# Kernel tuning notes

Measured on AMD Instinct MI355X. Metric: run time of the kernel, lower is better.

The kernel has to match this reference:

```python
import jax, jax.numpy as jnp
import numpy as np

EMBED_DIM = 1024
NUM_HEADS = 16
HEAD_DIM = EMBED_DIM // NUM_HEADS
BZ, Q_LEN, CACHE_LEN = 4, 512, 1536


def setup_inputs() -> dict:
    key = jax.random.key(0)
    ks = jax.random.split(key, 8)
    inp = {
        "hidden_states": jax.random.normal(ks[0], (BZ, Q_LEN, EMBED_DIM), jnp.float32),
        "attention_mask": jnp.zeros((BZ, 1, 1, CACHE_LEN + Q_LEN), jnp.float32),
        "k_cache": jax.random.normal(ks[1], (BZ, CACHE_LEN, EMBED_DIM), jnp.float32),
        "v_cache": jax.random.normal(ks[2], (BZ, CACHE_LEN, EMBED_DIM), jnp.float32),
        "Wq": jax.random.normal(ks[3], (EMBED_DIM, EMBED_DIM), jnp.float32) * 0.02,
        "bq": jnp.zeros((EMBED_DIM,), jnp.float32),
        "Wk": jax.random.normal(ks[4], (EMBED_DIM, EMBED_DIM), jnp.float32) * 0.02,
        "bk": jnp.zeros((EMBED_DIM,), jnp.float32),
        "Wv": jax.random.normal(ks[5], (EMBED_DIM, EMBED_DIM), jnp.float32) * 0.02,
        "bv": jnp.zeros((EMBED_DIM,), jnp.float32),
        "Wo": jax.random.normal(ks[6], (EMBED_DIM, EMBED_DIM), jnp.float32) * 0.02,
        "bo": jnp.zeros((EMBED_DIM,), jnp.float32),
    }
    return inp


def reference(hidden_states, attention_mask, k_cache, v_cache,
              Wq, bq, Wk, bk, Wv, bv, Wo, bo):
    bz, q_len, embed_dim = hidden_states.shape
    # projections (nn.Linear: x @ W.T + b)
    q = hidden_states @ Wq.T + bq
    k_new = hidden_states @ Wk.T + bk
    v_new = hidden_states @ Wv.T + bv
    # KV-cache concat (self_attn path)
    k = jnp.concatenate([k_cache, k_new], axis=1)  # [bz, kv_len, E]
    v = jnp.concatenate([v_cache, v_new], axis=1)
    q_begin = k_cache.shape[1]
    kv_len = k.shape[1]
    # split heads -> [bz, H, L, D]
    qh = q.reshape(bz, q_len, NUM_HEADS, HEAD_DIM).transpose(0, 2, 1, 3)
    kh = k.reshape(bz, kv_len, NUM_HEADS, HEAD_DIM).transpose(0, 2, 1, 3)
    vh = v.reshape(bz, kv_len, NUM_HEADS, HEAD_DIM).transpose(0, 2, 1, 3)
    scores = jnp.einsum("bhqd,bhkd->bhqk", qh, kh) / (HEAD_DIM ** 0.5)
    # causal mask slice causal_mask[q_begin:q_begin+q_len, :kv_len]
    rows = q_begin + jnp.arange(q_len)          # absolute query positions
    cols = jnp.arange(kv_len)
    causal = jnp.where(cols[None, :] > rows[:, None], -jnp.inf, 0.0).astype(scores.dtype)
    scores = scores + attention_mask + causal
    probs = jax.nn.softmax(scores, axis=-1)
    ctx = jnp.einsum("bhqk,bhkd->bhqd", probs, vh)
    ctx = ctx.transpose(0, 2, 1, 3).reshape(bz, q_len, embed_dim)
    out = ctx @ Wo.T + bo
    return out, k, v
```

## Files before the change

kernel.cpp:

```cpp
#include <hip/hip_runtime.h>
#include <hip/hip_bf16.h>
#include <stdint.h>

#define BZv 4
#define QL 512
#define CL 1536
#define KVL 2048
#define EMB 1024
#define NH 16
#define HD 64
#define QSCALE 0.18033688011112042f
#define NG 2048

typedef __attribute__((ext_vector_type(8))) short short8;
typedef __attribute__((ext_vector_type(4))) float floatx4;
typedef __attribute__((ext_vector_type(4))) float fx4;

__device__ __forceinline__ unsigned short f2b(float f) {
  union { float f; unsigned int u; } v; v.f = f;
  return (unsigned short)((v.u + 0x7FFFu + ((v.u >> 16) & 1u)) >> 16);
}

__device__ __forceinline__ ushort2 pk2(float a, float b) {
  union { __hip_bfloat162 h; ushort2 u; } c;
  c.h = __float22bfloat162_rn(make_float2(a, b));
  return c.u;
}

__device__ __forceinline__ short8 cvt8(fx4 a, fx4 b) {
  short8 r;
  r[0] = (short)f2b(a.x); r[1] = (short)f2b(a.y);
  r[2] = (short)f2b(a.z); r[3] = (short)f2b(a.w);
  r[4] = (short)f2b(b.x); r[5] = (short)f2b(b.y);
  r[6] = (short)f2b(b.z); r[7] = (short)f2b(b.w);
  return r;
}
__device__ __forceinline__ short8 cvt8w(fx4 a, fx4 b, float w) {
  short8 r;
  r[0] = (short)f2b(a.x * w); r[1] = (short)f2b(a.y * w);
  r[2] = (short)f2b(a.z * w); r[3] = (short)f2b(a.w * w);
  r[4] = (short)f2b(b.x * w); r[5] = (short)f2b(b.y * w);
  r[6] = (short)f2b(b.z * w); r[7] = (short)f2b(b.w * w);
  return r;
}

#if __has_builtin(__builtin_amdgcn_exp2f)
#define EXP2F(x) __builtin_amdgcn_exp2f(x)
#else
#define EXP2F(x) exp2f(x)
#endif

__device__ __forceinline__ void gload_lds16(const void* g, void* l) {
  __builtin_amdgcn_global_load_lds(
      (const __attribute__((address_space(1))) unsigned char*)g,
      (__attribute__((address_space(3))) unsigned char*)l, 16, 0, 0);
}

#define BAR_LIGHT() asm volatile("s_barrier" ::: "memory")
#define BAR_K() asm volatile("s_waitcnt vmcnt(3) lgkmcnt(0)\n\ts_barrier" ::: "memory")

__global__ __launch_bounds__(256) void prep_kernel(
    const float* __restrict__ hid, const float* __restrict__ Wq, const float* __restrict__ Wk,
    const float* __restrict__ Wv, const float* __restrict__ Wo,
    const float* __restrict__ kc, const float* __restrict__ vc, const float* __restrict__ msk,
    unsigned short* __restrict__ Xb, unsigned short* __restrict__ Wqb, unsigned short* __restrict__ Wkb,
    unsigned short* __restrict__ Wvb, unsigned short* __restrict__ Wob,
    unsigned short* __restrict__ Kb, unsigned short* __restrict__ Vb,
    float* __restrict__ kf, float* __restrict__ vf, unsigned short* __restrict__ wb)
{
  const int blk = blockIdx.x, tid = threadIdx.x;
  if (blk < 768) {
    const float* src; unsigned short* dst; int base;
    if (blk < 256) { src = hid; dst = Xb; base = blk * 2048; }
    else {
      int w = (blk - 256) >> 7, wo = (blk - 256) & 127;
      src = (w == 0) ? Wq : (w == 1) ? Wk : (w == 2) ? Wv : Wo;
      dst = (w == 0) ? Wqb : (w == 1) ? Wkb : (w == 2) ? Wvb : Wob;
      base = wo * 2048;
    }
    const fx4* s4 = (const fx4*)src;
    short8* d8 = (short8*)dst;
    fx4 v[8];
#pragma unroll
    for (int it = 0; it < 4; ++it) {
      int u = base + it * 512 + tid * 2;
      v[2 * it] = s4[u]; v[2 * it + 1] = s4[u + 1];
    }
#pragma unroll
    for (int it = 0; it < 4; ++it) {
      int u = base + it * 512 + tid * 2;
      d8[u >> 1] = cvt8(v[2 * it], v[2 * it + 1]);
    }
  } else if (blk < 1792) {
    const bool isV = blk >= 1280;
    const int r = blk - (isV ? 1280 : 768);
    const int bb = r >> 7, ko = r & 127;
    const fx4* s4 = (const fx4*)((isV ? vc : kc) + (long)bb * CL * EMB);
    fx4* f4 = (fx4*)((isV ? vf : kf) + (long)bb * KVL * EMB);
    short8* b8 = (short8*)((isV ? Vb : Kb) + (long)bb * KVL * EMB);
    const float* mrow = msk + bb * KVL;
    fx4 v[12];
#pragma unroll
    for (int it = 0; it < 6; ++it) {
      int u = ko * 3072 + it * 512 + tid * 2;
      v[2 * it] = s4[u]; v[2 * it + 1] = s4[u + 1];
    }
#pragma unroll
    for (int it = 0; it < 6; ++it) {
      int u = ko * 3072 + it * 512 + tid * 2;
      f4[u] = v[2 * it]; f4[u + 1] = v[2 * it + 1];
      if (isV) {
        float w = __expf(mrow[u >> 8]);
        b8[u >> 1] = cvt8w(v[2 * it], v[2 * it + 1], w);
      } else {
        b8[u >> 1] = cvt8(v[2 * it], v[2 * it + 1]);
      }
    }
  } else {
    const fx4* m4 = (const fx4*)msk;
    short8* w8 = (short8*)wb;
#pragma unroll
    for (int it = 0; it < 4; ++it) {
      int u = it * 512 + tid * 2;
      fx4 a = m4[u], b = m4[u + 1];
      fx4 ea, eb;
      ea.x = __expf(a.x); ea.y = __expf(a.y); ea.z = __expf(a.z); ea.w = __expf(a.w);
      eb.x = __expf(b.x); eb.y = __expf(b.y); eb.z = __expf(b.z); eb.w = __expf(b.w);
      w8[u >> 1] = cvt8(ea, eb);
    }
  }
}

__global__ __launch_bounds__(256) void qkv_gemm(
    const unsigned short* __restrict__ Xb,
    const unsigned short* __restrict__ Wqb, const unsigned short* __restrict__ Wkb,
    const unsigned short* __restrict__ Wvb,
    const float* __restrict__ bq, const float* __restrict__ bk, const float* __restrict__ bv,
    const float* __restrict__ msk,
    unsigned short* __restrict__ Qb, unsigned short* __restrict__ Kb, unsigned short* __restrict__ Vb,
    float* __restrict__ kf, float* __restrict__ vf)
{
  __shared__ unsigned short At[128 * 64];
  __shared__ unsigned short Bt[64 * 64];
  const int tid = threadIdx.x, lane = tid & 63, wave = tid >> 6;
  const int quad = lane >> 4, l = lane & 15;
  const int sw = l & 7;
  const int mat = blockIdx.x >> 4;
  const int ncol = (blockIdx.x & 15) * 64;
  const int mbase = blockIdx.y * 128;
  const unsigned short* W = (mat == 0) ? Wqb : (mat == 1) ? Wkb : Wvb;
  const float* bias = (mat == 0) ? bq : (mat == 1) ? bk : bv;
  const int rh = wave * 32;

  floatx4 zero = {0.f, 0.f, 0.f, 0.f};
  floatx4 acc[2][4];
#pragma unroll
  for (int i = 0; i < 2; i++)
#pragma unroll
    for (int j = 0; j < 4; j++) acc[i][j] = zero;

  for (int k0 = 0; k0 < EMB; k0 += 64) {
    if (k0) BAR_LIGHT();
#pragma unroll
    for (int s = 0; s < 4; s++) {
      int g = s * 256 + tid;
      int r = g >> 3, c = g & 7;
      gload_lds16(Xb + (size_t)(mbase + r) * EMB + k0 + ((c ^ (r & 7)) * 8), &At[g * 8]);
    }
#pragma unroll
    for (int s = 0; s < 2; s++) {
      int g = s * 256 + tid;
      int r = g >> 3, c = g & 7;
      gload_lds16(W + (size_t)(ncol + r) * EMB + k0 + ((c ^ (r & 7)) * 8), &Bt[g * 8]);
    }
    __syncthreads();
    short8 af[2][2], bfr[4][2];
#pragma unroll
    for (int rt = 0; rt < 2; rt++) {
      const unsigned short* p = &At[(rh + rt * 16 + l) * 64];
      af[rt][0] = *(const short8*)&p[(quad ^ sw) * 8];
      af[rt][1] = *(const short8*)&p[((quad + 4) ^ sw) * 8];
    }
#pragma unroll
    for (int ct = 0; ct < 4; ct++) {
      const unsigned short* p = &Bt[(ct * 16 + l) * 64];
      bfr[ct][0] = *(const short8*)&p[(quad ^ sw) * 8];
      bfr[ct][1] = *(const short8*)&p[((quad + 4) ^ sw) * 8];
    }
#pragma unroll
    for (int rt = 0; rt < 2; rt++)
#pragma unroll
      for (int ct = 0; ct < 4; ct++) {
        acc[rt][ct] = __builtin_amdgcn_mfma_f32_16x16x32_bf16(af[rt][0], bfr[ct][0], acc[rt][ct], 0, 0, 0);
        acc[rt][ct] = __builtin_amdgcn_mfma_f32_16x16x32_bf16(af[rt][1], bfr[ct][1], acc[rt][ct], 0, 0, 0);
      }
  }

#pragma unroll
  for (int ct = 0; ct < 4; ct++) {
    int col = ncol + ct * 16 + l;
    float bb = bias[col];
#pragma unroll
    for (int rt = 0; rt < 2; rt++)
#pragma unroll
      for (int r = 0; r < 4; r++) {
        int m = mbase + rh + rt * 16 + quad * 4 + r;
        float val = acc[rt][ct][r] + bb;
        if (mat == 0) {
          Qb[(size_t)m * EMB + col] = f2b(val * QSCALE);
        } else {
          size_t a = ((size_t)(m >> 9) * KVL + CL + (m & 511)) * EMB + col;
          if (mat == 1) { Kb[a] = f2b(val); kf[a] = val; }
          else {
            float w = __expf(msk[(m >> 9) * KVL + CL + (m & 511)]);
            Vb[a] = f2b(val * w); vf[a] = val;
          }
        }
      }
  }
}

__global__ __launch_bounds__(256) void oproj_gemm(
    const unsigned short* __restrict__ A, const unsigned short* __restrict__ W,
    const float* __restrict__ bias, float* __restrict__ out)
{
  __shared__ unsigned short At[64 * 64];
  __shared__ unsigned short Bt[64 * 64];
  const int tid = threadIdx.x, lane = tid & 63, wave = tid >> 6;
  const int quad = lane >> 4, l = lane & 15;
  const int sw = l & 7;
  const int ncol = blockIdx.x * 64;
  const int mbase = blockIdx.y * 64;
  const int rh = (wave & 1) * 32, ch = (wave >> 1) * 32;

  floatx4 zero = {0.f, 0.f, 0.f, 0.f};
  floatx4 acc[2][2];
#pragma unroll
  for (int i = 0; i < 2; i++)
#pragma unroll
    for (int j = 0; j < 2; j++) acc[i][j] = zero;

  for (int k0 = 0; k0 < EMB; k0 += 64) {
    if (k0) BAR_LIGHT();
#pragma unroll
    for (int s = 0; s < 2; s++) {
      int g = s * 256 + tid;
      int r = g >> 3, c = g & 7;
      gload_lds16(A + (size_t)(mbase + r) * EMB + k0 + ((c ^ (r & 7)) * 8), &At[g * 8]);
      gload_lds16(W + (size_t)(ncol + r) * EMB + k0 + ((c ^ (r & 7)) * 8), &Bt[g * 8]);
    }
    __syncthreads();
    short8 af[2][2], bfr[2][2];
#pragma unroll
    for (int rt = 0; rt < 2; rt++) {
      const unsigned short* p = &At[(rh + rt * 16 + l) * 64];
      af[rt][0] = *(const short8*)&p[(quad ^ sw) * 8];
      af[rt][1] = *(const short8*)&p[((quad + 4) ^ sw) * 8];
    }
#pragma unroll
    for (int ct = 0; ct < 2; ct++) {
      const unsigned short* p = &Bt[(ch + ct * 16 + l) * 64];
      bfr[ct][0] = *(const short8*)&p[(quad ^ sw) * 8];
      bfr[ct][1] = *(const short8*)&p[((quad + 4) ^ sw) * 8];
    }
#pragma unroll
    for (int rt = 0; rt < 2; rt++)
#pragma unroll
      for (int ct = 0; ct < 2; ct++) {
        acc[rt][ct] = __builtin_amdgcn_mfma_f32_16x16x32_bf16(af[rt][0], bfr[ct][0], acc[rt][ct], 0, 0, 0);
        acc[rt][ct] = __builtin_amdgcn_mfma_f32_16x16x32_bf16(af[rt][1], bfr[ct][1], acc[rt][ct], 0, 0, 0);
      }
  }

#pragma unroll
  for (int ct = 0; ct < 2; ct++) {
    int col = ncol + ch + ct * 16 + l;
    float bb = bias[col];
#pragma unroll
    for (int rt = 0; rt < 2; rt++)
#pragma unroll
      for (int r = 0; r < 4; r++) {
        int m = mbase + rh + rt * 16 + quad * 4 + r;
        out[(size_t)m * EMB + col] = acc[rt][ct][r] + bb;
      }
  }
}

__global__ __launch_bounds__(256, 4) void attn_kernel(
    const unsigned short* __restrict__ Qb, const unsigned short* __restrict__ Kb,
    const unsigned short* __restrict__ Vb, const unsigned short* __restrict__ wb,
    float* __restrict__ PO, float* __restrict__ PM, float* __restrict__ PD)
{
  __shared__ unsigned short Kt[2][64 * 64];
  __shared__ unsigned short Vt[65 * 72];
  __shared__ unsigned short Pl[4][16 * 72];

  const int bid = blockIdx.x;
  const int seg = bid >> 9;
  const int id = bid & 511;
  const int hb = id & 63, qt = id >> 6;
  const int b = hb >> 4, h = hb & 15;
  const int tid = threadIdx.x, lane = tid & 63, wave = tid >> 6;
  const int quad = lane >> 4, l = lane & 15;
  const int qbase = qt * 64 + wave * 16;

  const int nt_tot = (CL >> 6) + qt + 1;
  const int n0 = nt_tot >> 1;
  const int t_beg = seg ? n0 : 0;
  const int t_end = seg ? nt_tot : n0;

  const unsigned short* qp = Qb + (size_t)(b * QL + qbase + l) * EMB + h * HD + quad * 8;
  const short8 bq0 = *(const short8*)qp;
  const short8 bq1 = *(const short8*)(qp + 32);

  floatx4 zero = {0.f, 0.f, 0.f, 0.f};
  floatx4 o[4], o4 = zero;
#pragma unroll
  for (int c = 0; c < 4; c++) o[c] = zero;
  float mr = -INFINITY;

  const int vp = tid & 31, vg = tid >> 5;
  const unsigned short* vsrc = Vb + (size_t)(b * KVL) * EMB + h * HD + vg * 8;
  const unsigned short* wsrc = wb + (size_t)b * KVL + 2 * vp;
  const unsigned short* ksrc = Kb + (size_t)(b * KVL) * EMB + h * HD;
  const int sw = l & 7;

  uint4 va, vbr; ushort2 wn;
  auto VLOAD = [&](int t) {
    const unsigned short* vs = vsrc + (size_t)(t * 64 + 2 * vp) * EMB;
    va = *(const uint4*)vs;
    vbr = *(const uint4*)(vs + EMB);
    wn = *(const ushort2*)(wsrc + t * 64);
  };
  auto VSTAGE = [&]() {
    const unsigned short* pa = (const unsigned short*)&va;
    const unsigned short* pb = (const unsigned short*)&vbr;
#pragma unroll
    for (int j = 0; j < 8; j++) {
      ushort2 tt; tt.x = pa[j]; tt.y = pb[j];
      *(ushort2*)&Vt[(vg * 8 + j) * 72 + 2 * vp] = tt;
    }
    if (vg == 0) *(ushort2*)&Vt[64 * 72 + 2 * vp] = wn;
  };
  auto GLOAD_K = [&](int t, int buf) {
    const int kv0 = t * 64;
#pragma unroll
    for (int s = 0; s < 2; s++) {
      int g = s * 256 + tid;
      int r = g >> 3, k = g & 7;
      gload_lds16(ksrc + (size_t)(kv0 + r) * EMB + ((k ^ (r & 7)) * 8),
                  &Kt[buf][g * 8]);
    }
  };

  VLOAD(t_beg);
  GLOAD_K(t_beg, 0);
  __syncthreads();
  VSTAGE();
  if (t_beg + 1 < t_end) VLOAD(t_beg + 1);
  __syncthreads();

  int cur = 0;
  for (int t = t_beg; t < t_end; ++t) {
    if (t + 1 < t_end) GLOAD_K(t + 1, cur ^ 1);
    const int kv0 = t * 64;
    floatx4 s[4];
#pragma unroll
    for (int c = 0; c < 4; c++) {
      const int rr = c * 16 + l;
      const unsigned short* krow = &Kt[cur][rr * 64];
      short8 k0 = *(const short8*)&krow[(quad ^ sw) * 8];
      short8 k1 = *(const short8*)&krow[((quad + 4) ^ sw) * 8];
      s[c] = __builtin_amdgcn_mfma_f32_16x16x32_bf16(k0, bq0, zero, 0, 0, 0);
      s[c] = __builtin_amdgcn_mfma_f32_16x16x32_bf16(k1, bq1, s[c], 0, 0, 0);
    }
    if (kv0 + 63 > CL + qbase) {
      const int lim = CL + qbase + l;
#pragma unroll
      for (int c = 0; c < 4; c++) {
        int kvb = kv0 + c * 16 + quad * 4;
#pragma unroll
        for (int r = 0; r < 4; r++)
          s[c][r] = (kvb + r <= lim) ? s[c][r] : -INFINITY;
      }
    }
    float u0 = fmaxf(fmaxf(s[0][0], s[0][1]), fmaxf(s[0][2], s[0][3]));
    float u1 = fmaxf(fmaxf(s[1][0], s[1][1]), fmaxf(s[1][2], s[1][3]));
    float u2 = fmaxf(fmaxf(s[2][0], s[2][1]), fmaxf(s[2][2], s[2][3]));
    float u3 = fmaxf(fmaxf(s[3][0], s[3][1]), fmaxf(s[3][2], s[3][3]));
    float lmax = fmaxf(fmaxf(u0, u1), fmaxf(u2, u3));
    lmax = fmaxf(lmax, __shfl_xor(lmax, 16, 64));
    lmax = fmaxf(lmax, __shfl_xor(lmax, 32, 64));
    float mnew = fmaxf(mr, lmax);
    float alpha = EXP2F(mr - mnew);
    mr = mnew;
#pragma unroll
    for (int c = 0; c < 4; c++) {
      float p0 = EXP2F(s[c][0] - mnew), p1 = EXP2F(s[c][1] - mnew);
      float p2 = EXP2F(s[c][2] - mnew), p3 = EXP2F(s[c][3] - mnew);
      ushort2 lo = pk2(p0, p1), hi = pk2(p2, p3);
      ushort4 pk; pk.x = lo.x; pk.y = lo.y; pk.z = hi.x; pk.w = hi.y;
      *(ushort4*)&Pl[wave][l * 72 + c * 16 + quad * 4] = pk;
    }
#pragma unroll
    for (int c = 0; c < 4; c++)
#pragma unroll
      for (int r = 0; r < 4; r++) o[c][r] *= alpha;
#pragma unroll
    for (int r = 0; r < 4; r++) o4[r] *= alpha;
    asm volatile("s_waitcnt lgkmcnt(0)" ::: "memory");
    short8 pf0 = *(const short8*)&Pl[wave][l * 72 + quad * 8];
    short8 pf1 = *(const short8*)&Pl[wave][l * 72 + 32 + quad * 8];
    short8 vw0 = *(const short8*)&Vt[64 * 72 + quad * 8];
    short8 vw1 = *(const short8*)&Vt[64 * 72 + 32 + quad * 8];
    o4 = __builtin_amdgcn_mfma_f32_16x16x32_bf16(vw0, pf0, o4, 0, 0, 0);
    o4 = __builtin_amdgcn_mfma_f32_16x16x32_bf16(vw1, pf1, o4, 0, 0, 0);
#pragma unroll
    for (int c = 0; c < 4; c++) {
      short8 a0v = *(const short8*)&Vt[(c * 16 + l) * 72 + quad * 8];
      short8 a1v = *(const short8*)&Vt[(c * 16 + l) * 72 + 32 + quad * 8];
      o[c] = __builtin_amdgcn_mfma_f32_16x16x32_bf16(a0v, pf0, o[c], 0, 0, 0);
      o[c] = __builtin_amdgcn_mfma_f32_16x16x32_bf16(a1v, pf1, o[c], 0, 0, 0);
    }
    BAR_LIGHT();
    if (t + 1 < t_end) {
      VSTAGE();
      if (t + 2 < t_end) VLOAD(t + 2);
    }
    BAR_K();
    cur ^= 1;
  }

  const int gid = hb * 32 + qt * 4 + wave;
  float* po = PO + ((size_t)(seg * NG + gid)) * 1024 + l * 64;
#pragma unroll
  for (int c = 0; c < 4; c++)
    __builtin_nontemporal_store(o[c], (floatx4*)&po[c * 16 + quad * 4]);
  if (quad == 0) {
    __builtin_nontemporal_store(mr, &PM[(size_t)(seg * NG + gid) * 16 + l]);
    __builtin_nontemporal_store(o4[0], &PD[(size_t)(seg * NG + gid) * 16 + l]);
  }
}

__global__ __launch_bounds__(256) void attn_combine(
    const float* __restrict__ PO, const float* __restrict__ PM, const float* __restrict__ PD,
    unsigned short* __restrict__ Cb)
{
  const int tid = threadIdx.x, wave = tid >> 6, lane = tid & 63;
  const int quad = lane >> 4, l = lane & 15;
  const int gid = blockIdx.x * 4 + wave;
  const int hb = gid >> 5, qt = (gid >> 2) & 7, wv = gid & 3;
  const int b = hb >> 4, h = hb & 15;
  const int q = qt * 64 + wv * 16 + l;

  float m0 = __builtin_nontemporal_load(&PM[(size_t)gid * 16 + l]);
  float m1 = __builtin_nontemporal_load(&PM[(size_t)(NG + gid) * 16 + l]);
  float d0 = __builtin_nontemporal_load(&PD[(size_t)gid * 16 + l]);
  float d1 = __builtin_nontemporal_load(&PD[(size_t)(NG + gid) * 16 + l]);
  float M = fmaxf(m0, m1);
  float a0 = EXP2F(m0 - M), a1 = EXP2F(m1 - M);
  float inv = 1.0f / (d0 * a0 + d1 * a1);
  a0 *= inv; a1 *= inv;

  const fx4* p0 = (const fx4*)(PO + (size_t)gid * 1024 + l * 64 + quad * 16);
  const fx4* p1 = (const fx4*)((const float*)p0 + (size_t)NG * 1024);
  unsigned short* cp = Cb + (size_t)(b * QL + q) * EMB + h * HD + quad * 16;
#pragma unroll
  for (int v = 0; v < 4; v++) {
    fx4 x0 = __builtin_nontemporal_load(p0 + v);
    fx4 x1 = __builtin_nontemporal_load(p1 + v);
    ushort4 w4;
    w4.x = f2b(x0.x * a0 + x1.x * a1);
    w4.y = f2b(x0.y * a0 + x1.y * a1);
    w4.z = f2b(x0.z * a0 + x1.z * a1);
    w4.w = f2b(x0.w * a0 + x1.w * a1);
    *(ushort4*)(cp + v * 4) = w4;
  }
}

extern "C" void kernel_launch(void* const* d_in, const int* in_sizes, int n_in,
                              void* d_out, int out_size, void* d_ws, size_t ws_size,
                              hipStream_t stream) {
  const float* hid  = (const float*)d_in[0];
  const float* mask = (const float*)d_in[1];
  const float* kc   = (const float*)d_in[2];
  const float* vc   = (const float*)d_in[3];
  const float* Wq   = (const float*)d_in[4];
  const float* bq   = (const float*)d_in[5];
  const float* Wk   = (const float*)d_in[6];
  const float* bk   = (const float*)d_in[7];
  const float* Wv   = (const float*)d_in[8];
  const float* bv   = (const float*)d_in[9];
  const float* Wo   = (const float*)d_in[10];
  const float* bo   = (const float*)d_in[11];

  float* out_f = (float*)d_out;
  float* kf = out_f + (size_t)BZv * QL * EMB;
  float* vf = kf + (size_t)BZv * KVL * EMB;

  char* p = (char*)d_ws;
  unsigned short* Xb  = (unsigned short*)p; p += (size_t)BZv * QL * EMB * 2;
  unsigned short* Wqb = (unsigned short*)p; p += (size_t)EMB * EMB * 2;
  unsigned short* Wkb = (unsigned short*)p; p += (size_t)EMB * EMB * 2;
  unsigned short* Wvb = (unsigned short*)p; p += (size_t)EMB * EMB * 2;
  unsigned short* Wob = (unsigned short*)p; p += (size_t)EMB * EMB * 2;
  unsigned short* Qb  = (unsigned short*)p; p += (size_t)BZv * QL * EMB * 2;
  unsigned short* Kb  = (unsigned short*)p; p += (size_t)BZv * KVL * EMB * 2;
  unsigned short* Vb  = (unsigned short*)p; p += (size_t)BZv * KVL * EMB * 2;
  unsigned short* Cb  = (unsigned short*)p; p += (size_t)BZv * QL * EMB * 2;
  unsigned short* wbp = (unsigned short*)p; p += (size_t)BZv * KVL * 2;
  float* POp = (float*)p; p += (size_t)2 * NG * 1024 * 4;
  float* PMp = (float*)p; p += (size_t)2 * NG * 16 * 4;
  float* PDp = (float*)p; p += (size_t)2 * NG * 16 * 4;

  prep_kernel<<<1793, 256, 0, stream>>>(hid, Wq, Wk, Wv, Wo, kc, vc, mask,
                                        Xb, Wqb, Wkb, Wvb, Wob, Kb, Vb, kf, vf, wbp);
  qkv_gemm<<<dim3(48, 16), 256, 0, stream>>>(Xb, Wqb, Wkb, Wvb, bq, bk, bv, mask,
                                             Qb, Kb, Vb, kf, vf);
  attn_kernel<<<1024, 256, 0, stream>>>(Qb, Kb, Vb, wbp, POp, PMp, PDp);
  attn_combine<<<512, 256, 0, stream>>>(POp, PMp, PDp, Cb);
  oproj_gemm<<<dim3(16, 32), 256, 0, stream>>>(Cb, Wob, bo, out_f);
}
```

Before: 237.7 us.

## Split attention KV range into three segments and pass P via shuffles

The attention kernel now splits each query tile's KV range into three segments instead of two, launching 1536 blocks, and the combine kernel merges three partial results. The softmax probabilities are also moved from the per-wave LDS staging buffer into registers via cross-lane shuffles, which removes the LDS write/read round trip and its waitcnt. This gives more parallelism and lower LDS use, at the cost of more partial-output traffic, extra combine work and many shuffle instructions per tile.

```diff
diff --git a/kernel.cpp b/kernel.cpp
--- a/kernel.cpp
+++ b/kernel.cpp
@@ -11,6 +11,7 @@
 #define HD 64
 #define QSCALE 0.18033688011112042f
 #define NG 2048
+#define NSEG 3
 
 typedef __attribute__((ext_vector_type(8))) short short8;
 typedef __attribute__((ext_vector_type(4))) float floatx4;
@@ -21,8 +22,8 @@
   return (unsigned short)((v.u + 0x7FFFu + ((v.u >> 16) & 1u)) >> 16);
 }
 
-__device__ __forceinline__ ushort2 pk2(float a, float b) {
-  union { __hip_bfloat162 h; ushort2 u; } c;
+__device__ __forceinline__ unsigned pku(float a, float b) {
+  union { __hip_bfloat162 h; unsigned u; } c;
   c.h = __float22bfloat162_rn(make_float2(a, b));
   return c.u;
 }
@@ -293,7 +294,6 @@
 {
   __shared__ unsigned short Kt[2][64 * 64];
   __shared__ unsigned short Vt[65 * 72];
-  __shared__ unsigned short Pl[4][16 * 72];
 
   const int bid = blockIdx.x;
   const int seg = bid >> 9;
@@ -305,9 +305,9 @@
   const int qbase = qt * 64 + wave * 16;
 
   const int nt_tot = (CL >> 6) + qt + 1;
-  const int n0 = nt_tot >> 1;
-  const int t_beg = seg ? n0 : 0;
-  const int t_end = seg ? nt_tot : n0;
+  const int n1 = nt_tot / 3, n2 = (2 * nt_tot) / 3;
+  const int t_beg = (seg == 0) ? 0 : (seg == 1) ? n1 : n2;
+  const int t_end = (seg == 0) ? n1 : (seg == 1) ? n2 : nt_tot;
 
   const unsigned short* qp = Qb + (size_t)(b * QL + qbase + l) * EMB + h * HD + quad * 8;
   const short8 bq0 = *(const short8*)qp;
@@ -360,6 +360,9 @@
   if (t_beg + 1 < t_end) VLOAD(t_beg + 1);
   __syncthreads();
 
+  const int la = 32 * (quad & 1) + l;
+  const bool chi = (quad & 2) != 0;
+
   int cur = 0;
   for (int t = t_beg; t < t_end; ++t) {
     if (t + 1 < t_end) GLOAD_K(t + 1, cur ^ 1);
@@ -394,13 +397,12 @@
     float mnew = fmaxf(mr, lmax);
     float alpha = EXP2F(mr - mnew);
     mr = mnew;
+    unsigned plo[4], phi[4];
 #pragma unroll
     for (int c = 0; c < 4; c++) {
       float p0 = EXP2F(s[c][0] - mnew), p1 = EXP2F(s[c][1] - mnew);
       float p2 = EXP2F(s[c][2] - mnew), p3 = EXP2F(s[c][3] - mnew);
-      ushort2 lo = pk2(p0, p1), hi = pk2(p2, p3);
-      ushort4 pk; pk.x = lo.x; pk.y = lo.y; pk.z = hi.x; pk.w = hi.y;
-      *(ushort4*)&Pl[wave][l * 72 + c * 16 + quad * 4] = pk;
+      plo[c] = pku(p0, p1); phi[c] = pku(p2, p3);
     }
 #pragma unroll
     for (int c = 0; c < 4; c++)
@@ -408,9 +410,20 @@
       for (int r = 0; r < 4; r++) o[c][r] *= alpha;
 #pragma unroll
     for (int r = 0; r < 4; r++) o4[r] *= alpha;
-    asm volatile("s_waitcnt lgkmcnt(0)" ::: "memory");
-    short8 pf0 = *(const short8*)&Pl[wave][l * 72 + quad * 8];
-    short8 pf1 = *(const short8*)&Pl[wave][l * 72 + 32 + quad * 8];
+    unsigned a0 = (unsigned)__shfl((int)plo[0], la), a1 = (unsigned)__shfl((int)plo[1], la);
+    unsigned b0 = (unsigned)__shfl((int)phi[0], la), b1 = (unsigned)__shfl((int)phi[1], la);
+    unsigned c0 = (unsigned)__shfl((int)plo[0], la + 16), c1 = (unsigned)__shfl((int)plo[1], la + 16);
+    unsigned d0 = (unsigned)__shfl((int)phi[0], la + 16), d1 = (unsigned)__shfl((int)phi[1], la + 16);
+    unsigned e0 = (unsigned)__shfl((int)plo[2], la), e1 = (unsigned)__shfl((int)plo[3], la);
+    unsigned f0 = (unsigned)__shfl((int)phi[2], la), f1 = (unsigned)__shfl((int)phi[3], la);
+    unsigned g0 = (unsigned)__shfl((int)plo[2], la + 16), g1 = (unsigned)__shfl((int)plo[3], la + 16);
+    unsigned h0 = (unsigned)__shfl((int)phi[2], la + 16), h1 = (unsigned)__shfl((int)phi[3], la + 16);
+    union { unsigned u[4]; short8 s8; } P0, P1;
+    P0.u[0] = chi ? a1 : a0;  P0.u[1] = chi ? b1 : b0;
+    P0.u[2] = chi ? c1 : c0;  P0.u[3] = chi ? d1 : d0;
+    P1.u[0] = chi ? e1 : e0;  P1.u[1] = chi ? f1 : f0;
+    P1.u[2] = chi ? g1 : g0;  P1.u[3] = chi ? h1 : h0;
+    short8 pf0 = P0.s8, pf1 = P1.s8;
     short8 vw0 = *(const short8*)&Vt[64 * 72 + quad * 8];
     short8 vw1 = *(const short8*)&Vt[64 * 72 + 32 + quad * 8];
     o4 = __builtin_amdgcn_mfma_f32_16x16x32_bf16(vw0, pf0, o4, 0, 0, 0);
@@ -455,25 +468,29 @@
 
   float m0 = __builtin_nontemporal_load(&PM[(size_t)gid * 16 + l]);
   float m1 = __builtin_nontemporal_load(&PM[(size_t)(NG + gid) * 16 + l]);
+  float m2 = __builtin_nontemporal_load(&PM[(size_t)(2 * NG + gid) * 16 + l]);
   float d0 = __builtin_nontemporal_load(&PD[(size_t)gid * 16 + l]);
   float d1 = __builtin_nontemporal_load(&PD[(size_t)(NG + gid) * 16 + l]);
-  float M = fmaxf(m0, m1);
-  float a0 = EXP2F(m0 - M), a1 = EXP2F(m1 - M);
-  float inv = 1.0f / (d0 * a0 + d1 * a1);
-  a0 *= inv; a1 *= inv;
+  float d2 = __builtin_nontemporal_load(&PD[(size_t)(2 * NG + gid) * 16 + l]);
+  float M = fmaxf(m0, fmaxf(m1, m2));
+  float a0 = EXP2F(m0 - M), a1 = EXP2F(m1 - M), a2 = EXP2F(m2 - M);
+  float inv = 1.0f / (d0 * a0 + d1 * a1 + d2 * a2);
+  a0 *= inv; a1 *= inv; a2 *= inv;
 
   const fx4* p0 = (const fx4*)(PO + (size_t)gid * 1024 + l * 64 + quad * 16);
   const fx4* p1 = (const fx4*)((const float*)p0 + (size_t)NG * 1024);
+  const fx4* p2 = (const fx4*)((const float*)p0 + (size_t)2 * NG * 1024);
   unsigned short* cp = Cb + (size_t)(b * QL + q) * EMB + h * HD + quad * 16;
 #pragma unroll
   for (int v = 0; v < 4; v++) {
     fx4 x0 = __builtin_nontemporal_load(p0 + v);
     fx4 x1 = __builtin_nontemporal_load(p1 + v);
+    fx4 x2 = __builtin_nontemporal_load(p2 + v);
     ushort4 w4;
-    w4.x = f2b(x0.x * a0 + x1.x * a1);
-    w4.y = f2b(x0.y * a0 + x1.y * a1);
-    w4.z = f2b(x0.z * a0 + x1.z * a1);
-    w4.w = f2b(x0.w * a0 + x1.w * a1);
+    w4.x = f2b(x0.x * a0 + x1.x * a1 + x2.x * a2);
+    w4.y = f2b(x0.y * a0 + x1.y * a1 + x2.y * a2);
+    w4.z = f2b(x0.z * a0 + x1.z * a1 + x2.z * a2);
+    w4.w = f2b(x0.w * a0 + x1.w * a1 + x2.w * a2);
     *(ushort4*)(cp + v * 4) = w4;
   }
 }
@@ -509,15 +526,15 @@
   unsigned short* Vb  = (unsigned short*)p; p += (size_t)BZv * KVL * EMB * 2;
   unsigned short* Cb  = (unsigned short*)p; p += (size_t)BZv * QL * EMB * 2;
   unsigned short* wbp = (unsigned short*)p; p += (size_t)BZv * KVL * 2;
-  float* POp = (float*)p; p += (size_t)2 * NG * 1024 * 4;
-  float* PMp = (float*)p; p += (size_t)2 * NG * 16 * 4;
-  float* PDp = (float*)p; p += (size_t)2 * NG * 16 * 4;
+  float* POp = (float*)p; p += (size_t)NSEG * NG * 1024 * 4;
+  float* PMp = (float*)p; p += (size_t)NSEG * NG * 16 * 4;
+  float* PDp = (float*)p; p += (size_t)NSEG * NG * 16 * 4;
 
   prep_kernel<<<1793, 256, 0, stream>>>(hid, Wq, Wk, Wv, Wo, kc, vc, mask,
                                         Xb, Wqb, Wkb, Wvb, Wob, Kb, Vb, kf, vf, wbp);
   qkv_gemm<<<dim3(48, 16), 256, 0, stream>>>(Xb, Wqb, Wkb, Wvb, bq, bk, bv, mask,
                                              Qb, Kb, Vb, kf, vf);
-  attn_kernel<<<1024, 256, 0, stream>>>(Qb, Kb, Vb, wbp, POp, PMp, PDp);
+  attn_kernel<<<NSEG * 512, 256, 0, stream>>>(Qb, Kb, Vb, wbp, POp, PMp, PDp);
   attn_combine<<<512, 256, 0, stream>>>(POp, PMp, PDp, Cb);
   oproj_gemm<<<dim3(16, 32), 256, 0, stream>>>(Cb, Wob, bo, out_f);
 }
```

After: 248.2 us. 4.4% more time.
